# Kernel tuning notes

Measured on AMD Instinct MI355X. Metric: run time of the kernel, lower is better.

Reference implementation:

```python
import jax, jax.numpy as jnp
import numpy as np

B, NQ, NK, DQ, DK, DV, H = 4, 512, 512, 512, 512, 512, 128
NEG_INF = -1e20


def setup_inputs() -> dict:
    key = jax.random.key(0)
    ks = jax.random.split(key, 7)
    Q = jax.random.normal(ks[0], (B, NQ, DQ), dtype=jnp.float32)
    K = jax.random.normal(ks[1], (B, NK, DK), dtype=jnp.float32)
    V = jax.random.normal(ks[2], (B, NK, DV), dtype=jnp.float32)
    # learned params (LazyLinear, bias=False): y = x @ W with W[in, out]
    Wq = jax.random.normal(ks[3], (DQ, H), dtype=jnp.float32) / np.sqrt(DQ)
    Wk = jax.random.normal(ks[4], (DK, H), dtype=jnp.float32) / np.sqrt(DK)
    wv = jax.random.normal(ks[5], (H,), dtype=jnp.float32) / np.sqrt(H)
    valid_lens = jax.random.randint(ks[6], (B,), 1, NK + 1).astype(jnp.int64)
    return {"Q": Q, "K": K, "V": V, "Wq": Wq, "Wk": Wk, "wv": wv,
            "valid_lens": valid_lens}


def reference(Q, K, V, Wq, Wk, wv, valid_lens):
    # Project queries and keys to shared hidden size H
    Qp = Q @ Wq                      # (B, NQ, H)
    Kp = K @ Wk                      # (B, NK, H)
    # Additive (Bahdanau) broadcast: (B, NQ, NK, H)
    S = jnp.tanh(Qp[:, :, None, :] + Kp[:, None, :, :])
    # Linear score to scalar: (B, NQ, NK)
    scores = jnp.einsum('bqkh,h->bqk', S, wv)
    # Mask positions k >= valid_lens[b] (1-D valid_lens broadcast over queries)
    kv_idx = jnp.arange(scores.shape[-1])[None, None, :]
    mask = kv_idx < valid_lens[:, None, None]
    scores = jnp.where(mask, scores, NEG_INF)
    W = jax.nn.softmax(scores, axis=-1)  # dropout rate 0.0 -> identity
    return jnp.einsum('bqk,bkv->bqv', W, V)
```

## Files before the change

kernel.cpp:

```cpp
#include <hip/hip_runtime.h>

#define B_   4
#define NQ_  512
#define NK_  512
#define D_   512
#define H_   128

typedef __attribute__((ext_vector_type(8))) short short8;
typedef __attribute__((ext_vector_type(8))) unsigned short ushort8;
typedef __attribute__((ext_vector_type(4))) float f32x4;

__device__ __forceinline__ float fexp2(float x) { return __builtin_amdgcn_exp2f(x); }
__device__ __forceinline__ float frcp(float x)  { return __builtin_amdgcn_rcpf(x); }
__device__ __forceinline__ unsigned short f2bf(float f) {
    unsigned int u = __builtin_bit_cast(unsigned int, f);
    u += 0x7FFFu + ((u >> 16) & 1u);
    return (unsigned short)(u >> 16);
}
__device__ __forceinline__ float bf2f(unsigned short h) {
    return __builtin_bit_cast(float, (unsigned int)h << 16);
}


#define WS_EQK   0
#define WS_WP    524288
#define WS_WBF   524544
#define WS_VT    1048832

__global__ __launch_bounds__(512, 4) void projvt_kernel(
    const float* __restrict__ Q, const float* __restrict__ K,
    const float* __restrict__ Wq, const float* __restrict__ Wk,
    const float* __restrict__ V, const float* __restrict__ wv,
    const int* __restrict__ valid_lens,
    float* __restrict__ wp, unsigned short* __restrict__ Vt,
    float* __restrict__ Eqk)
{
    __shared__ __align__(16) unsigned short smem_u[2 * 32 * 520];
    const int t  = threadIdx.x;
    const int bx = blockIdx.x;

    if (bx >= 128) {
        const int id = bx - 128;
        const int kt = id & 7, dt = (id >> 3) & 7, b = id >> 6;
        const int vl = valid_lens[b];

        if (kt * 64 >= ((vl + 127) & ~127)) return;

        if (kt * 64 >= vl) {
            #pragma unroll
            for (int p = 0; p < 2; ++p) {
                const int idx = p * 512 + t;
                const int d  = idx >> 4;
                const int k4 = (idx & 15) * 4;
                ushort4 z; z.x = 0; z.y = 0; z.z = 0; z.w = 0;
                *reinterpret_cast<ushort4*>(
                    Vt + ((size_t)b * D_ + dt * 64 + d) * NK_ + kt * 64 + k4) = z;
            }
            return;
        }

        float (*Vl)[69] = (float(*)[69])smem_u;

        #pragma unroll
        for (int p = 0; p < 2; ++p) {
            const int idx = p * 512 + t;
            const int r  = idx >> 4;
            const int c4 = (idx & 15) * 4;
            const float4 v = *reinterpret_cast<const float4*>(
                V + ((size_t)b * NK_ + kt * 64 + r) * D_ + dt * 64 + c4);
            Vl[r][c4 + 0] = v.x; Vl[r][c4 + 1] = v.y;
            Vl[r][c4 + 2] = v.z; Vl[r][c4 + 3] = v.w;
        }
        __syncthreads();

        #pragma unroll
        for (int p = 0; p < 2; ++p) {
            const int idx = p * 512 + t;
            const int d  = idx >> 4;
            const int k4 = (idx & 15) * 4;
            ushort4 o;
            o.x = f2bf(Vl[k4 + 0][d]); o.y = f2bf(Vl[k4 + 1][d]);
            o.z = f2bf(Vl[k4 + 2][d]); o.w = f2bf(Vl[k4 + 3][d]);
            *reinterpret_cast<ushort4*>(
                Vt + ((size_t)b * D_ + dt * 64 + d) * NK_ + kt * 64 + k4) = o;
        }
        return;
    }

    if (bx == 0 && t < 64) {
        const float2 w2 = reinterpret_cast<const float2*>(wv)[t];
        const float wn0 = -2.0f * w2.x;
        const float wn1 = -2.0f * w2.y;
        reinterpret_cast<float4*>(wp)[t] =
            make_float4(wn0, wn1, wn0 + wn1, 0.0f);
    }

    const bool isQ = bx < 64;
    const int xr0  = isQ ? bx * 32 : (bx - 64) * 32;
    if (!isQ) {
        const int kr = xr0 & 511;
        const int bb = xr0 >> 9;
        if (kr >= valid_lens[bb]) return;
    }
    const float* __restrict__ X  = isQ ? Q : K;
    const float* __restrict__ Wm = isQ ? Wq : Wk;
    const int er0 = isQ ? xr0 : 2048 + xr0;

    unsigned short (*Ahi)[520] = (unsigned short(*)[520])smem_u;
    unsigned short (*Alo)[520] = (unsigned short(*)[520])(smem_u + 32 * 520);

    #pragma unroll
    for (int p = 0; p < 8; ++p) {
        const int idx = p * 512 + t;
        const int row = idx >> 7;
        const int kq  = (idx & 127) * 4;
        const float4 v = *reinterpret_cast<const float4*>(
            X + (size_t)(xr0 + row) * D_ + kq);
        ushort4 h, l;
        h.x = f2bf(v.x); l.x = f2bf(v.x - bf2f(h.x));
        h.y = f2bf(v.y); l.y = f2bf(v.y - bf2f(h.y));
        h.z = f2bf(v.z); l.z = f2bf(v.z - bf2f(h.z));
        h.w = f2bf(v.w); l.w = f2bf(v.w - bf2f(h.w));
        *reinterpret_cast<ushort4*>(&Ahi[row][kq]) = h;
        *reinterpret_cast<ushort4*>(&Alo[row][kq]) = l;
    }
    __syncthreads();

    const int wave = __builtin_amdgcn_readfirstlane(t >> 6);
    const int lane = t & 63;
    const int m    = lane & 15;
    const int quad = lane >> 4;
    const int col  = wave * 16 + m;
    const float* __restrict__ Wcol = Wm + col;

    f32x4 a0A = {0.f,0.f,0.f,0.f}, a0B = {0.f,0.f,0.f,0.f};
    f32x4 a1A = {0.f,0.f,0.f,0.f}, a1B = {0.f,0.f,0.f,0.f};

    #pragma unroll 2
    for (int ksg = 0; ksg < 16; ++ksg) {
        const int k0 = ksg * 32 + quad * 8;
        float wr[8];
        #pragma unroll
        for (int j = 0; j < 8; ++j)
            wr[j] = Wcol[(size_t)(k0 + j) * H_];
        short8 bh, bl;
        #pragma unroll
        for (int j = 0; j < 8; ++j) {
            const unsigned short h = f2bf(wr[j]);
            bh[j] = (short)h;
            bl[j] = (short)f2bf(wr[j] - bf2f(h));
        }
        const short8 ah0 = *reinterpret_cast<const short8*>(&Ahi[     m][k0]);
        const short8 al0 = *reinterpret_cast<const short8*>(&Alo[     m][k0]);
        const short8 ah1 = *reinterpret_cast<const short8*>(&Ahi[16 + m][k0]);
        const short8 al1 = *reinterpret_cast<const short8*>(&Alo[16 + m][k0]);
        f32x4& A0 = (ksg & 1) ? a0B : a0A;
        f32x4& A1 = (ksg & 1) ? a1B : a1A;
        A0 = __builtin_amdgcn_mfma_f32_16x16x32_bf16(ah0, bh, A0, 0, 0, 0);
        A0 = __builtin_amdgcn_mfma_f32_16x16x32_bf16(al0, bh, A0, 0, 0, 0);
        A0 = __builtin_amdgcn_mfma_f32_16x16x32_bf16(ah0, bl, A0, 0, 0, 0);
        A1 = __builtin_amdgcn_mfma_f32_16x16x32_bf16(ah1, bh, A1, 0, 0, 0);
        A1 = __builtin_amdgcn_mfma_f32_16x16x32_bf16(al1, bh, A1, 0, 0, 0);
        A1 = __builtin_amdgcn_mfma_f32_16x16x32_bf16(ah1, bl, A1, 0, 0, 0);
    }

    const float C2 = 2.88539008177792681472f;
    #pragma unroll
    for (int i = 0; i < 4; ++i) {
        Eqk[(size_t)(er0 + quad * 4 + i) * H_ + col] =
            fexp2(C2 * (a0A[i] + a0B[i]));
        Eqk[(size_t)(er0 + 16 + quad * 4 + i) * H_ + col] =
            fexp2(C2 * (a1A[i] + a1B[i]));
    }
}

__global__ __launch_bounds__(512, 4) void score_softmax_kernel(
    const float* __restrict__ Eqk, const float* __restrict__ wp,
    const int* __restrict__ valid_lens, unsigned short* __restrict__ Wbf)
{
    const int rb   = blockIdx.x;
    const int t    = threadIdx.x;
    const int w    = __builtin_amdgcn_readfirstlane(t >> 6);
    const int lane = t & 63;
    const int rloc = w >> 1;
    const int half = w & 1;
    const int row  = rb * 4 + rloc;
    const int b    = row >> 9;

    __shared__ __align__(16) float4 Ks[2 * 64 * 33];
    __shared__ float redM[4][2], redS[4][2];

    const int vl = valid_lens[b];

    const float4* __restrict__ Q4 =
        reinterpret_cast<const float4*>(Eqk + (size_t)row * H_);
    const float4* __restrict__ wp4 = reinterpret_cast<const float4*>(wp);
    const float4* __restrict__ Kp4 =
        reinterpret_cast<const float4*>(Eqk + (size_t)(2048 + b * NK_) * H_);

    float vals[4];

    for (int c = 0; c < 4; ++c) {
        if (c) __syncthreads();
        #pragma unroll
        for (int p = 0; p < 8; ++p) {
            const int hh = p >> 2;
            if (hh * 256 + c * 64 < vl) {
                const int r  = (p & 3) * 16 + (t >> 5);
                const int h4 = t & 31;
                Ks[(hh * 64 + r) * 33 + h4] =
                    Kp4[(size_t)(hh * 256 + c * 64 + r) * 32 + h4];
            }
        }
        __syncthreads();

        float s = 0.0f;
        if (half * 256 + c * 64 < vl) {
            #pragma unroll 4
            for (int g = 0; g < 32; ++g) {
                const float4 kv = Ks[(half * 64 + lane) * 33 + g];
                const float4 qa = Q4[g];
                const float4 wa = wp4[2 * g];
                const float4 wb = wp4[2 * g + 1];
                const float e0 = qa.x * kv.x;
                const float e1 = qa.y * kv.y;
                const float e2 = qa.z * kv.z;
                const float e3 = qa.w * kv.w;
                const float D01 = 1.0f + fmaf(e0, e1, e0 + e1);
                const float D23 = 1.0f + fmaf(e2, e3, e2 + e3);
                const float n01 = fmaf(wa.y, e0, fmaf(wa.x, e1, wa.z));
                const float n23 = fmaf(wb.y, e2, fmaf(wb.x, e3, wb.z));
                const float N   = fmaf(n23, D01, n01 * D23);
                s = fmaf(N, frcp(D01 * D23), s);
            }
        }
        vals[c] = s;
    }

    const float L2E = 1.44269504088896340736f;
    float m = -1e30f;
    #pragma unroll
    for (int c = 0; c < 4; ++c) {
        const int k = half * 256 + c * 64 + lane;
        vals[c] = (k < vl) ? vals[c] : -1e30f;
        m = fmaxf(m, vals[c]);
    }
    #pragma unroll
    for (int off = 32; off >= 1; off >>= 1)
        m = fmaxf(m, __shfl_xor(m, off, 64));
    float sum = 0.0f;
    #pragma unroll
    for (int c = 0; c < 4; ++c)
        sum += fexp2((vals[c] - m) * L2E);
    #pragma unroll
    for (int off = 32; off >= 1; off >>= 1)
        sum += __shfl_xor(sum, off, 64);

    if (lane == 0) { redM[rloc][half] = m; redS[rloc][half] = sum; }
    __syncthreads();

    const float m0 = redM[rloc][0], m1 = redM[rloc][1];
    const float s0 = redS[rloc][0], s1 = redS[rloc][1];
    const float M  = fmaxf(m0, m1);
    const float S  = fmaf(s0, fexp2((m0 - M) * L2E),
                          s1 * fexp2((m1 - M) * L2E));
    const float inv = frcp(S);

    unsigned short* __restrict__ dst = Wbf + (size_t)row * NK_ + half * 256;
    #pragma unroll
    for (int c = 0; c < 4; ++c)
        dst[c * 64 + lane] = f2bf(fexp2((vals[c] - M) * L2E) * inv);
}

__global__ __launch_bounds__(256) void av_gemm_kernel(
    const unsigned short* __restrict__ Wbf, const unsigned short* __restrict__ Vt,
    const int* __restrict__ valid_lens, float* __restrict__ O)
{
    const int c0 = blockIdx.x * 64;
    const int r0 = blockIdx.y * 64;
    const int b  = blockIdx.z;
    const int t  = threadIdx.x;
    const int wave = __builtin_amdgcn_readfirstlane(t >> 6);
    const int lane = t & 63;
    const int m    = lane & 15;
    const int quad = lane >> 4;

    const int vl = valid_lens[b];

    __shared__ unsigned short Al [64][136];
    __shared__ unsigned short Btl[64][136];

    f32x4 acc0 = {0.f,0.f,0.f,0.f}, acc1 = {0.f,0.f,0.f,0.f};
    f32x4 acc2 = {0.f,0.f,0.f,0.f}, acc3 = {0.f,0.f,0.f,0.f};

    for (int kc = 0; kc < 4; ++kc) {
        if (kc * 128 >= vl) break;
        if (kc) __syncthreads();
        #pragma unroll
        for (int p = 0; p < 4; ++p) {
            const int idx = p * 256 + t;
            const int rl = idx >> 4;
            const int k8 = (idx & 15) * 8;
            *reinterpret_cast<uint4*>(&Al[rl][k8]) =
                *reinterpret_cast<const uint4*>(
                    Wbf + ((size_t)b * NQ_ + r0 + rl) * NK_ + kc * 128 + k8);
            *reinterpret_cast<uint4*>(&Btl[rl][k8]) =
                *reinterpret_cast<const uint4*>(
                    Vt + ((size_t)b * D_ + c0 + rl) * NK_ + kc * 128 + k8);
        }
        __syncthreads();

        #pragma unroll
        for (int sub = 0; sub < 4; ++sub) {
            const int kcol = sub * 32 + quad * 8;
            const short8 a = *reinterpret_cast<const short8*>(&Al[wave * 16 + m][kcol]);
            const short8 b0 = *reinterpret_cast<const short8*>(&Btl[ 0 + m][kcol]);
            const short8 b1 = *reinterpret_cast<const short8*>(&Btl[16 + m][kcol]);
            const short8 b2 = *reinterpret_cast<const short8*>(&Btl[32 + m][kcol]);
            const short8 b3 = *reinterpret_cast<const short8*>(&Btl[48 + m][kcol]);
            acc0 = __builtin_amdgcn_mfma_f32_16x16x32_bf16(a, b0, acc0, 0, 0, 0);
            acc1 = __builtin_amdgcn_mfma_f32_16x16x32_bf16(a, b1, acc1, 0, 0, 0);
            acc2 = __builtin_amdgcn_mfma_f32_16x16x32_bf16(a, b2, acc2, 0, 0, 0);
            acc3 = __builtin_amdgcn_mfma_f32_16x16x32_bf16(a, b3, acc3, 0, 0, 0);
        }
    }

    const size_t rowbase = (size_t)b * NQ_ + r0 + wave * 16 + quad * 4;
    #pragma unroll
    for (int i = 0; i < 4; ++i) {
        float* __restrict__ orow = O + (rowbase + i) * D_ + c0 + m;
        orow[ 0] = acc0[i];
        orow[16] = acc1[i];
        orow[32] = acc2[i];
        orow[48] = acc3[i];
    }
}

extern "C" void kernel_launch(void* const* d_in, const int* in_sizes, int n_in,
                              void* d_out, int out_size, void* d_ws, size_t ws_size,
                              hipStream_t stream) {
    (void)in_sizes; (void)n_in; (void)out_size; (void)ws_size;

    const float* Q   = (const float*)d_in[0];
    const float* K   = (const float*)d_in[1];
    const float* V   = (const float*)d_in[2];
    const float* Wq  = (const float*)d_in[3];
    const float* Wk  = (const float*)d_in[4];
    const float* wv  = (const float*)d_in[5];
    const int*   vl  = (const int*)d_in[6];
    float* out = (float*)d_out;

    float* ws  = (float*)d_ws;
    float* Eqk = ws + WS_EQK;
    float* wp  = ws + WS_WP;
    unsigned short* Wbf = (unsigned short*)(ws + WS_WBF);
    unsigned short* Vt  = (unsigned short*)(ws + WS_VT);

    projvt_kernel<<<dim3(384), 512, 0, stream>>>(Q, K, Wq, Wk, V, wv, vl,
                                                 wp, Vt, Eqk);
    score_softmax_kernel<<<dim3(512), 512, 0, stream>>>(Eqk, wp, vl, Wbf);
    av_gemm_kernel<<<dim3(8, 8, 4), 256, 0, stream>>>(Wbf, Vt, vl, out);
}
```

Baseline: 110.0 us.

## Fuse softmax and AV GEMM into one kernel with LDS-resident weights

Merges the score/softmax kernel and the separate attention-times-V GEMM. The normalized bf16 weights for the block's 4 query rows are kept in shared memory, reusing the Ks buffer, and each wave multiplies them against its 64 columns of Vt read straight from global memory with MFMA. This removes one kernel launch and the global round trip of the weight matrix. In exchange, each block re-reads the whole Vt slice for its batch from L2/HBM without shared-memory reuse, and the 16-row MFMA tiles carry only 4 useful rows.

After: 118.6 us. 7.9% more time.

```diff
diff --git a/kernel.cpp b/kernel.cpp
--- a/kernel.cpp
+++ b/kernel.cpp
@@ -24,7 +24,6 @@
 
 #define WS_EQK   0
 #define WS_WP    524288
-#define WS_WBF   524544
 #define WS_VT    1048832
 
 __global__ __launch_bounds__(512, 4) void projvt_kernel(
@@ -174,9 +173,10 @@
     }
 }
 
-__global__ __launch_bounds__(512, 4) void score_softmax_kernel(
+__global__ __launch_bounds__(512, 4) void score_av_kernel(
     const float* __restrict__ Eqk, const float* __restrict__ wp,
-    const int* __restrict__ valid_lens, unsigned short* __restrict__ Wbf)
+    const int* __restrict__ valid_lens,
+    const unsigned short* __restrict__ Vt, float* __restrict__ O)
 {
     const int rb   = blockIdx.x;
     const int t    = threadIdx.x;
@@ -189,6 +189,7 @@
 
     __shared__ __align__(16) float4 Ks[2 * 64 * 33];
     __shared__ float redM[4][2], redS[4][2];
+    unsigned short (*Wl)[520] = (unsigned short(*)[520])Ks;
 
     const int vl = valid_lens[b];
 
@@ -266,73 +267,46 @@
                           s1 * fexp2((m1 - M) * L2E));
     const float inv = frcp(S);
 
-    unsigned short* __restrict__ dst = Wbf + (size_t)row * NK_ + half * 256;
+    unsigned short* __restrict__ wrow = &Wl[rloc][half * 256];
     #pragma unroll
     for (int c = 0; c < 4; ++c)
-        dst[c * 64 + lane] = f2bf(fexp2((vals[c] - M) * L2E) * inv);
-}
-
-__global__ __launch_bounds__(256) void av_gemm_kernel(
-    const unsigned short* __restrict__ Wbf, const unsigned short* __restrict__ Vt,
-    const int* __restrict__ valid_lens, float* __restrict__ O)
-{
-    const int c0 = blockIdx.x * 64;
-    const int r0 = blockIdx.y * 64;
-    const int b  = blockIdx.z;
-    const int t  = threadIdx.x;
-    const int wave = __builtin_amdgcn_readfirstlane(t >> 6);
-    const int lane = t & 63;
-    const int m    = lane & 15;
+        wrow[c * 64 + lane] = f2bf(fexp2((vals[c] - M) * L2E) * inv);
+    __syncthreads();
+
+    const int mm   = lane & 15;
     const int quad = lane >> 4;
-
-    const int vl = valid_lens[b];
-
-    __shared__ unsigned short Al [64][136];
-    __shared__ unsigned short Btl[64][136];
+    const unsigned short* __restrict__ Vb0 =
+        Vt + ((size_t)b * D_ + w * 64 +  0 + mm) * NK_;
+    const unsigned short* __restrict__ Vb1 = Vb0 + 16 * NK_;
+    const unsigned short* __restrict__ Vb2 = Vb0 + 32 * NK_;
+    const unsigned short* __restrict__ Vb3 = Vb0 + 48 * NK_;
 
     f32x4 acc0 = {0.f,0.f,0.f,0.f}, acc1 = {0.f,0.f,0.f,0.f};
     f32x4 acc2 = {0.f,0.f,0.f,0.f}, acc3 = {0.f,0.f,0.f,0.f};
 
-    for (int kc = 0; kc < 4; ++kc) {
-        if (kc * 128 >= vl) break;
-        if (kc) __syncthreads();
-        #pragma unroll
-        for (int p = 0; p < 4; ++p) {
-            const int idx = p * 256 + t;
-            const int rl = idx >> 4;
-            const int k8 = (idx & 15) * 8;
-            *reinterpret_cast<uint4*>(&Al[rl][k8]) =
-                *reinterpret_cast<const uint4*>(
-                    Wbf + ((size_t)b * NQ_ + r0 + rl) * NK_ + kc * 128 + k8);
-            *reinterpret_cast<uint4*>(&Btl[rl][k8]) =
-                *reinterpret_cast<const uint4*>(
-                    Vt + ((size_t)b * D_ + c0 + rl) * NK_ + kc * 128 + k8);
-        }
-        __syncthreads();
-
-        #pragma unroll
-        for (int sub = 0; sub < 4; ++sub) {
-            const int kcol = sub * 32 + quad * 8;
-            const short8 a = *reinterpret_cast<const short8*>(&Al[wave * 16 + m][kcol]);
-            const short8 b0 = *reinterpret_cast<const short8*>(&Btl[ 0 + m][kcol]);
-            const short8 b1 = *reinterpret_cast<const short8*>(&Btl[16 + m][kcol]);
-            const short8 b2 = *reinterpret_cast<const short8*>(&Btl[32 + m][kcol]);
-            const short8 b3 = *reinterpret_cast<const short8*>(&Btl[48 + m][kcol]);
-            acc0 = __builtin_amdgcn_mfma_f32_16x16x32_bf16(a, b0, acc0, 0, 0, 0);
-            acc1 = __builtin_amdgcn_mfma_f32_16x16x32_bf16(a, b1, acc1, 0, 0, 0);
-            acc2 = __builtin_amdgcn_mfma_f32_16x16x32_bf16(a, b2, acc2, 0, 0, 0);
-            acc3 = __builtin_amdgcn_mfma_f32_16x16x32_bf16(a, b3, acc3, 0, 0, 0);
-        }
-    }
-
-    const size_t rowbase = (size_t)b * NQ_ + r0 + wave * 16 + quad * 4;
-    #pragma unroll
-    for (int i = 0; i < 4; ++i) {
-        float* __restrict__ orow = O + (rowbase + i) * D_ + c0 + m;
-        orow[ 0] = acc0[i];
-        orow[16] = acc1[i];
-        orow[32] = acc2[i];
-        orow[48] = acc3[i];
+    const int nk = (vl + 31) >> 5;
+    for (int kc = 0; kc < nk; ++kc) {
+        const int k0 = kc * 32 + quad * 8;
+        const short8 a  = *reinterpret_cast<const short8*>(&Wl[mm][k0]);
+        const short8 b0 = *reinterpret_cast<const short8*>(Vb0 + k0);
+        const short8 b1 = *reinterpret_cast<const short8*>(Vb1 + k0);
+        const short8 b2 = *reinterpret_cast<const short8*>(Vb2 + k0);
+        const short8 b3 = *reinterpret_cast<const short8*>(Vb3 + k0);
+        acc0 = __builtin_amdgcn_mfma_f32_16x16x32_bf16(a, b0, acc0, 0, 0, 0);
+        acc1 = __builtin_amdgcn_mfma_f32_16x16x32_bf16(a, b1, acc1, 0, 0, 0);
+        acc2 = __builtin_amdgcn_mfma_f32_16x16x32_bf16(a, b2, acc2, 0, 0, 0);
+        acc3 = __builtin_amdgcn_mfma_f32_16x16x32_bf16(a, b3, acc3, 0, 0, 0);
+    }
+
+    if (quad == 0) {
+        #pragma unroll
+        for (int i = 0; i < 4; ++i) {
+            float* __restrict__ orow = O + (size_t)(rb * 4 + i) * D_ + w * 64 + mm;
+            orow[ 0] = acc0[i];
+            orow[16] = acc1[i];
+            orow[32] = acc2[i];
+            orow[48] = acc3[i];
+        }
     }
 }
 
@@ -353,11 +327,9 @@
     float* ws  = (float*)d_ws;
     float* Eqk = ws + WS_EQK;
     float* wp  = ws + WS_WP;
-    unsigned short* Wbf = (unsigned short*)(ws + WS_WBF);
     unsigned short* Vt  = (unsigned short*)(ws + WS_VT);
 
     projvt_kernel<<<dim3(384), 512, 0, stream>>>(Q, K, Wq, Wk, V, wv, vl,
                                                  wp, Vt, Eqk);
-    score_softmax_kernel<<<dim3(512), 512, 0, stream>>>(Eqk, wp, vl, Wbf);
-    av_gemm_kernel<<<dim3(8, 8, 4), 256, 0, stream>>>(Wbf, Vt, vl, out);
-}
+    score_av_kernel<<<dim3(512), 512, 0, stream>>>(Eqk, wp, vl, Vt, out);
+}
```

## Prefetch next K chunk into registers and interleave batches across block indices

Applied to the files above, without the earlier changes.

The score kernel now loads the next 64-row chunk of projected keys into registers while the current chunk is written to LDS, so global loads overlap with compute. Both the score and AV kernels remap block indices so consecutive blocks cycle through batches. Because valid_lens differs per batch, this spreads short and long batches evenly across CUs and reduces tail imbalance. The prefetch buffer costs extra registers per thread, which could lower occupancy.

Result: slower. 136.7 us (+24.3%).

```diff
diff --git a/kernel.cpp b/kernel.cpp
--- a/kernel.cpp
+++ b/kernel.cpp
@@ -184,8 +184,8 @@
     const int lane = t & 63;
     const int rloc = w >> 1;
     const int half = w & 1;
-    const int row  = rb * 4 + rloc;
-    const int b    = row >> 9;
+    const int b    = rb & 3;
+    const int row  = b * 512 + (rb >> 2) * 4 + rloc;
 
     __shared__ __align__(16) float4 Ks[2 * 64 * 33];
     __shared__ float redM[4][2], redS[4][2];
@@ -198,6 +198,19 @@
     const float4* __restrict__ Kp4 =
         reinterpret_cast<const float4*>(Eqk + (size_t)(2048 + b * NK_) * H_);
 
+    const int sr = (t >> 5);
+    const int h4 = t & 31;
+
+    float4 pr[8];
+    #pragma unroll
+    for (int p = 0; p < 8; ++p) {
+        const int hh = p >> 2;
+        if (hh * 256 < vl) {
+            const int r = (p & 3) * 16 + sr;
+            pr[p] = Kp4[(size_t)(hh * 256 + r) * 32 + h4];
+        }
+    }
+
     float vals[4];
 
     for (int c = 0; c < 4; ++c) {
@@ -206,10 +219,18 @@
         for (int p = 0; p < 8; ++p) {
             const int hh = p >> 2;
             if (hh * 256 + c * 64 < vl) {
-                const int r  = (p & 3) * 16 + (t >> 5);
-                const int h4 = t & 31;
-                Ks[(hh * 64 + r) * 33 + h4] =
-                    Kp4[(size_t)(hh * 256 + c * 64 + r) * 32 + h4];
+                const int r = (p & 3) * 16 + sr;
+                Ks[(hh * 64 + r) * 33 + h4] = pr[p];
+            }
+        }
+        if (c < 3) {
+            #pragma unroll
+            for (int p = 0; p < 8; ++p) {
+                const int hh = p >> 2;
+                if (hh * 256 + (c + 1) * 64 < vl) {
+                    const int r = (p & 3) * 16 + sr;
+                    pr[p] = Kp4[(size_t)(hh * 256 + (c + 1) * 64 + r) * 32 + h4];
+                }
             }
         }
         __syncthreads();
@@ -276,9 +297,10 @@
     const unsigned short* __restrict__ Wbf, const unsigned short* __restrict__ Vt,
     const int* __restrict__ valid_lens, float* __restrict__ O)
 {
-    const int c0 = blockIdx.x * 64;
+    const int bx = blockIdx.x;
+    const int b  = bx & 3;
+    const int c0 = (bx >> 2) * 64;
     const int r0 = blockIdx.y * 64;
-    const int b  = blockIdx.z;
     const int t  = threadIdx.x;
     const int wave = __builtin_amdgcn_readfirstlane(t >> 6);
     const int lane = t & 63;
@@ -359,5 +381,5 @@
     projvt_kernel<<<dim3(384), 512, 0, stream>>>(Q, K, Wq, Wk, V, wv, vl,
                                                  wp, Vt, Eqk);
     score_softmax_kernel<<<dim3(512), 512, 0, stream>>>(Eqk, wp, vl, Wbf);
-    av_gemm_kernel<<<dim3(8, 8, 4), 256, 0, stream>>>(Wbf, Vt, vl, out);
-}
+    av_gemm_kernel<<<dim3(32, 8), 256, 0, stream>>>(Wbf, Vt, vl, out);
+}
```
